# Performance work log

Measured on AMD Instinct MI355X. Metric: run time of the kernel, lower is better.

The kernel has to match this reference:

```python
import jax, jax.numpy as jnp
import numpy as np

DIM = 1536
DEPTH = 8
HEADS = 8
KV_HEADS = 1
GROUPS = HEADS // KV_HEADS
DQK = 128
DV = 192
DIM_PW = 128
POOL = 16
FF_INNER = int(DIM * 2.0)
SOFTCLAMP = 5.0
SCALE = 64 ** -0.5  # source uses default dim_head=64 for scale, not dim_head_qk
MAX_POS = 8192
EPS = float(jnp.finfo(jnp.float32).eps)


def rmsnorm(x, g):
    return x * jax.lax.rsqrt(jnp.mean(x * x, axis=-1, keepdims=True) + EPS) * g


def rotate_half(x):
    x1, x2 = jnp.split(x, 2, axis=-1)
    return jnp.concatenate([-x2, x1], axis=-1)


def apply_rope(pos, t):
    return t * jnp.cos(pos) + rotate_half(t) * jnp.sin(pos)


def rotary_emb(seq_len):
    nf = DQK // 2
    # torch.logspace(1, MAX_POS-nf+1, nf) = 10**linspace -> overflows to inf in fp32 (faithful)
    inv_freq = 1.0 / (jnp.arange(nf, dtype=jnp.float32) + 10.0 ** jnp.linspace(1.0, MAX_POS - nf + 1, nf, dtype=jnp.float32))
    freqs = jnp.arange(seq_len, dtype=jnp.float32)[:, None] * inv_freq[None, :]
    return jnp.concatenate([freqs, freqs], axis=-1)  # [n, DQK]


def softclamp(t, value=SOFTCLAMP):
    return jnp.tanh(t / value) * value


def attention(x, pairwise, rope, w_qkv, qg, kg, vg, bg, w_bias, w_out):
    b, n, _ = x.shape
    qkv = x @ w_qkv
    q, k, v = jnp.split(qkv, [HEADS * DQK, HEADS * DQK + DQK], axis=-1)
    # b n (g h d) -> b g h n d
    q = q.reshape(b, n, GROUPS, KV_HEADS, DQK).transpose(0, 2, 3, 1, 4)
    k = k.reshape(b, n, KV_HEADS, DQK).transpose(0, 2, 1, 3)
    v = v.reshape(b, n, KV_HEADS, DV).transpose(0, 2, 1, 3)
    q = rmsnorm(q, qg)
    k = rmsnorm(k, kg)
    v = rmsnorm(v, vg)
    q = q * SCALE
    q = apply_rope(rope, q)
    k = apply_rope(rope, k)
    sim = jnp.einsum('bghid,bhjd->bghij', q, k)
    # pairwise bias: RMSNorm -> GELU -> Linear(dim_pw, heads) -> b g h i j
    pb = jax.nn.gelu(rmsnorm(pairwise, bg), approximate=False) @ w_bias  # [b, i, j, heads]
    bi = pb.shape[1]
    bias = pb.reshape(b, bi, bi, GROUPS, KV_HEADS).transpose(0, 3, 4, 1, 2)
    bias = jnp.repeat(jnp.repeat(bias, POOL, axis=3), POOL, axis=4)  # expand to seq res
    sim = softclamp(sim + bias)
    attn = jax.nn.softmax(sim, axis=-1)
    out = jnp.einsum('bghij,bhjd->bghid', attn, v)
    out = out.transpose(0, 3, 1, 2, 4).reshape(b, n, GROUPS * KV_HEADS * DV)
    return out @ w_out


def tower(x, pairwise, w_qkv, q_gamma, k_gamma, v_gamma, bias_gamma, w_bias, w_out, attn_pre_gamma, ff_pre_gamma, w_ff1, b_ff1, w_ff2, b_ff2):
    rope = rotary_emb(x.shape[1])
    for d in range(DEPTH):
        xn = rmsnorm(x, attn_pre_gamma[d])
        x = x + attention(xn, pairwise, rope, w_qkv[d], q_gamma[d], k_gamma[d], v_gamma[d], bias_gamma[d], w_bias[d], w_out[d])
        xn = rmsnorm(x, ff_pre_gamma[d])
        x = x + (jax.nn.relu(xn @ w_ff1[d] + b_ff1[d]) @ w_ff2[d] + b_ff2[d])
    return x


def setup_inputs() -> dict:
    key = jax.random.key(0)
    ks = jax.random.split(key, 10)
    s = 0.02
    inp = {
        'x': jax.random.normal(ks[0], (2, 2048, DIM), jnp.float32),
        'pairwise': jax.random.normal(ks[1], (2, 128, 128, DIM_PW), jnp.float32),
        'w_qkv': jax.random.normal(ks[2], (DEPTH, DIM, HEADS * DQK + DQK + DV), jnp.float32) * s,
        'q_gamma': jnp.ones((DEPTH, DQK), jnp.float32),
        'k_gamma': jnp.ones((DEPTH, DQK), jnp.float32),
        'v_gamma': jnp.ones((DEPTH, DV), jnp.float32),
        'bias_gamma': jnp.ones((DEPTH, DIM_PW), jnp.float32),
        'w_bias': jax.random.normal(ks[3], (DEPTH, DIM_PW, HEADS), jnp.float32) * s,
        'w_out': jax.random.normal(ks[4], (DEPTH, DV * HEADS, DIM), jnp.float32) * s,
        'attn_pre_gamma': jnp.ones((DEPTH, DIM), jnp.float32),
        'ff_pre_gamma': jnp.ones((DEPTH, DIM), jnp.float32),
        'w_ff1': jax.random.normal(ks[5], (DEPTH, DIM, FF_INNER), jnp.float32) * s,
        'b_ff1': jnp.zeros((DEPTH, FF_INNER), jnp.float32),
        'w_ff2': jax.random.normal(ks[6], (DEPTH, FF_INNER, DIM), jnp.float32) * s,
        'b_ff2': jnp.zeros((DEPTH, DIM), jnp.float32),
    }
    return inp


def reference(x, pairwise, w_qkv, q_gamma, k_gamma, v_gamma, bias_gamma, w_bias, w_out, attn_pre_gamma, ff_pre_gamma, w_ff1, b_ff1, w_ff2, b_ff2):
    return tower(x, pairwise, w_qkv, q_gamma, k_gamma, v_gamma, bias_gamma, w_bias, w_out, attn_pre_gamma, ff_pre_gamma, w_ff1, b_ff1, w_ff2, b_ff2)
```

## Files before the change

### kernel.cpp

```cpp
#include <hip/hip_runtime.h>

typedef __bf16 bf16;
typedef float f32x4 __attribute__((ext_vector_type(4)));
typedef __bf16 bf16x8 __attribute__((ext_vector_type(8)));
typedef __bf16 bf16x4 __attribute__((ext_vector_type(4)));

#define EPSF 1.1920928955078125e-07f

#define GLOAD_LDS16(gsrc, ldst) \
  __builtin_amdgcn_global_load_lds((const __attribute__((address_space(1))) void*)(gsrc), \
                                   (__attribute__((address_space(3))) void*)(ldst), 16, 0, 0)

__device__ __forceinline__ float wave_reduce_sum(float v) {
#pragma unroll
  for (int m = 1; m < 64; m <<= 1) v += __shfl_xor(v, m, 64);
  return v;
}

__global__ __launch_bounds__(256) void wcast_t(const float* __restrict__ src,
                                               bf16* __restrict__ dst, int R, int C) {
  __shared__ float t[32][33];
  int z = blockIdx.z;
  const float* s = src + (size_t)z * R * C;
  bf16* d = dst + (size_t)z * R * C;
  int c0 = blockIdx.x * 32, r0 = blockIdx.y * 32;
  int tx = threadIdx.x, ty = threadIdx.y;
#pragma unroll
  for (int k = 0; k < 4; ++k)
    t[ty + k * 8][tx] = s[(size_t)(r0 + ty + k * 8) * C + c0 + tx];
  __syncthreads();
#pragma unroll
  for (int k = 0; k < 4; ++k)
    d[(size_t)(c0 + ty + k * 8) * R + r0 + tx] = (bf16)t[tx][ty + k * 8];
}

__global__ __launch_bounds__(256) void rmsnorm_k(const float* __restrict__ X,
                                                 const float* __restrict__ G,
                                                 bf16* __restrict__ O) {
  int row = blockIdx.x, tid = threadIdx.x, lane = tid & 63, w = tid >> 6;
  const float* x = X + (size_t)row * 1536;
  float v[6];
  float ss = 0.f;
#pragma unroll
  for (int k = 0; k < 6; ++k) { v[k] = x[tid + k * 256]; ss += v[k] * v[k]; }
  ss = wave_reduce_sum(ss);
  __shared__ float wsum[4];
  if (lane == 0) wsum[w] = ss;
  __syncthreads();
  ss = wsum[0] + wsum[1] + wsum[2] + wsum[3];
  float rs = rsqrtf(ss * (1.f / 1536.f) + EPSF);
  bf16* o = O + (size_t)row * 1536;
#pragma unroll
  for (int k = 0; k < 6; ++k) o[tid + k * 256] = (bf16)(v[k] * rs * G[tid + k * 256]);
}

template <int EPI>
__global__ __launch_bounds__(256, 3) void gemm_bt(const bf16* __restrict__ A,
                                                  const bf16* __restrict__ Bt,
                                                  float* __restrict__ Cf,
                                                  bf16* __restrict__ Cb,
                                                  const float* __restrict__ bias,
                                                  int M, int N, int K) {
  __shared__ __align__(16) char As[128 * 128];
  __shared__ __align__(16) char Bs[128 * 128];
  const int tid = threadIdx.x;
  const int lane = tid & 63, l15 = lane & 15, l4 = lane >> 4;
  const int w = tid >> 6;
  const int nwg = gridDim.x * gridDim.y;
  const int bid = blockIdx.y * gridDim.x + blockIdx.x;
  const int cpx = nwg >> 3;
  const int swz = (bid & 7) * cpx + (bid >> 3);
  const int rm = (swz / gridDim.x) * 128;
  const int cn = (swz % gridDim.x) * 128;
  const int wm = (w >> 1) * 64, wn = (w & 1) * 64;
  f32x4 acc[4][4] = {};

  for (int kk = 0; kk < K; kk += 64) {
#pragma unroll
    for (int r = 0; r < 4; ++r) {
      uint32_t o = (uint32_t)(r * 256 + tid) * 16;
      uint32_t row = o >> 7;
      uint32_t kb = ((o >> 4) & 7) ^ (row & 7);
      const bf16* src = A + (size_t)(rm + (int)row) * K + kk + kb * 8;
      GLOAD_LDS16(src, As + (o & 0xFFFFFC00u));
    }
#pragma unroll
    for (int r = 0; r < 4; ++r) {
      uint32_t o = (uint32_t)(r * 256 + tid) * 16;
      uint32_t row = o >> 7;
      uint32_t kb = ((o >> 4) & 7) ^ (row & 7);
      int nrow = cn + (int)row;
      if (nrow >= N) nrow = N - 1;
      const bf16* src = Bt + (size_t)nrow * K + kk + kb * 8;
      GLOAD_LDS16(src, Bs + (o & 0xFFFFFC00u));
    }
    __syncthreads();
#pragma unroll
    for (int s = 0; s < 2; ++s) {
      bf16x8 a[4], b[4];
#pragma unroll
      for (int m = 0; m < 4; ++m) {
        uint32_t row = wm + m * 16 + l15;
        uint32_t kb = (uint32_t)(s * 4 + l4);
        a[m] = *(const bf16x8*)(As + row * 128 + (kb ^ (row & 7)) * 16);
      }
#pragma unroll
      for (int n = 0; n < 4; ++n) {
        uint32_t row = wn + n * 16 + l15;
        uint32_t kb = (uint32_t)(s * 4 + l4);
        b[n] = *(const bf16x8*)(Bs + row * 128 + (kb ^ (row & 7)) * 16);
      }
      __builtin_amdgcn_s_setprio(1);
#pragma unroll
      for (int m = 0; m < 4; ++m)
#pragma unroll
        for (int n = 0; n < 4; ++n)
          acc[m][n] = __builtin_amdgcn_mfma_f32_16x16x32_bf16(a[m], b[n], acc[m][n], 0, 0, 0);
      __builtin_amdgcn_s_setprio(0);
    }
    __syncthreads();
  }

#pragma unroll
  for (int m = 0; m < 4; ++m)
#pragma unroll
    for (int n = 0; n < 4; ++n)
#pragma unroll
      for (int r = 0; r < 4; ++r) {
        int row = rm + wm + m * 16 + l4 * 4 + r;
        int col = cn + wn + n * 16 + l15;
        if (col < N) {
          float v = acc[m][n][r];
          size_t idx = (size_t)row * N + col;
          if constexpr (EPI == 0) {
            Cf[idx] = v;
          } else if constexpr (EPI == 2) {
            Cf[idx] += v;
          } else if constexpr (EPI == 3) {
            float tv = v + bias[col];
            Cb[idx] = (bf16)(tv > 0.f ? tv : 0.f);
          } else if constexpr (EPI == 4) {
            Cf[idx] += v + bias[col];
          }
        }
      }
}

template <int EPI>
__global__ __launch_bounds__(256, 4) void gemm_bt64(const bf16* __restrict__ A,
                                                    const bf16* __restrict__ Bt,
                                                    float* __restrict__ Cf,
                                                    bf16* __restrict__ Cb,
                                                    const float* __restrict__ bias,
                                                    int M, int N, int K) {
  __shared__ __align__(16) char As[64 * 128];
  __shared__ __align__(16) char Bs[128 * 128];
  const int tid = threadIdx.x;
  const int lane = tid & 63, l15 = lane & 15, l4 = lane >> 4;
  const int w = tid >> 6;
  const int nwg = gridDim.x * gridDim.y;
  const int bid = blockIdx.y * gridDim.x + blockIdx.x;
  const int cpx = nwg >> 3;
  const int swz = (bid & 7) * cpx + (bid >> 3);
  const int rm = (swz / gridDim.x) * 64;
  const int cn = (swz % gridDim.x) * 128;
  const int wm = (w >> 1) * 32, wn = (w & 1) * 64;
  f32x4 acc[2][4] = {};

  for (int kk = 0; kk < K; kk += 64) {
#pragma unroll
    for (int r = 0; r < 2; ++r) {
      uint32_t o = (uint32_t)(r * 256 + tid) * 16;
      uint32_t row = o >> 7;
      uint32_t kb = ((o >> 4) & 7) ^ (row & 7);
      const bf16* src = A + (size_t)(rm + (int)row) * K + kk + kb * 8;
      GLOAD_LDS16(src, As + (o & 0xFFFFFC00u));
    }
#pragma unroll
    for (int r = 0; r < 4; ++r) {
      uint32_t o = (uint32_t)(r * 256 + tid) * 16;
      uint32_t row = o >> 7;
      uint32_t kb = ((o >> 4) & 7) ^ (row & 7);
      int nrow = cn + (int)row;
      if (nrow >= N) nrow = N - 1;
      const bf16* src = Bt + (size_t)nrow * K + kk + kb * 8;
      GLOAD_LDS16(src, Bs + (o & 0xFFFFFC00u));
    }
    __syncthreads();
#pragma unroll
    for (int s = 0; s < 2; ++s) {
      bf16x8 a[2], b[4];
#pragma unroll
      for (int m = 0; m < 2; ++m) {
        uint32_t row = wm + m * 16 + l15;
        uint32_t kb = (uint32_t)(s * 4 + l4);
        a[m] = *(const bf16x8*)(As + row * 128 + (kb ^ (row & 7)) * 16);
      }
#pragma unroll
      for (int n = 0; n < 4; ++n) {
        uint32_t row = wn + n * 16 + l15;
        uint32_t kb = (uint32_t)(s * 4 + l4);
        b[n] = *(const bf16x8*)(Bs + row * 128 + (kb ^ (row & 7)) * 16);
      }
      __builtin_amdgcn_s_setprio(1);
#pragma unroll
      for (int m = 0; m < 2; ++m)
#pragma unroll
        for (int n = 0; n < 4; ++n)
          acc[m][n] = __builtin_amdgcn_mfma_f32_16x16x32_bf16(a[m], b[n], acc[m][n], 0, 0, 0);
      __builtin_amdgcn_s_setprio(0);
    }
    __syncthreads();
  }

#pragma unroll
  for (int m = 0; m < 2; ++m)
#pragma unroll
    for (int n = 0; n < 4; ++n)
#pragma unroll
      for (int r = 0; r < 4; ++r) {
        int row = rm + wm + m * 16 + l4 * 4 + r;
        int col = cn + wn + n * 16 + l15;
        if (col < N) {
          float v = acc[m][n][r];
          size_t idx = (size_t)row * N + col;
          if constexpr (EPI == 0) {
            Cf[idx] = v;
          } else if constexpr (EPI == 2) {
            Cf[idx] += v;
          } else if constexpr (EPI == 3) {
            float tv = v + bias[col];
            Cb[idx] = (bf16)(tv > 0.f ? tv : 0.f);
          } else if constexpr (EPI == 4) {
            Cf[idx] += v + bias[col];
          }
        }
      }
}

__global__ void qkv_post(const float* __restrict__ qkv, const float* __restrict__ qg,
                         const float* __restrict__ kg, const float* __restrict__ vg,
                         bf16* __restrict__ Qo, bf16* __restrict__ Ko, bf16* __restrict__ Vo) {
  int t = blockIdx.x, seg = blockIdx.y, lane = threadIdx.x;
  int b = t >> 11, n = t & 2047;
  const float* base;
  const float* gamma;
  int len;
  if (seg < 8) { base = qkv + (size_t)t * 1344 + seg * 128; gamma = qg; len = 128; }
  else if (seg == 8) { base = qkv + (size_t)t * 1344 + 1024; gamma = kg; len = 128; }
  else { base = qkv + (size_t)t * 1344 + 1152; gamma = vg; len = 192; }
  float v0 = base[lane], v1 = base[lane + 64];
  float v2 = (len == 192) ? base[lane + 128] : 0.f;
  float ss = wave_reduce_sum(v0 * v0 + v1 * v1 + v2 * v2);
  float rs = rsqrtf(ss / (float)len + EPSF);
  float n0 = v0 * rs * gamma[lane];
  float n1 = v1 * rs * gamma[lane + 64];
  if (seg < 8) {
    n0 *= 0.125f; n1 *= 0.125f;
    if (lane == 0) {
      float th = 0.1f * (float)n;
      float c = cosf(th), s_ = sinf(th);
      float r0 = n0 * c - n1 * s_, r1 = n1 * c + n0 * s_;
      n0 = r0; n1 = r1;
    }
    bf16* q = Qo + ((size_t)((b * 8 + seg) * 2048 + n)) * 128;
    q[lane] = (bf16)n0; q[lane + 64] = (bf16)n1;
  } else if (seg == 8) {
    if (lane == 0) {
      float th = 0.1f * (float)n;
      float c = cosf(th), s_ = sinf(th);
      float r0 = n0 * c - n1 * s_, r1 = n1 * c + n0 * s_;
      n0 = r0; n1 = r1;
    }
    bf16* k = Ko + ((size_t)(b * 2048 + n)) * 128;
    k[lane] = (bf16)n0; k[lane + 64] = (bf16)n1;
  } else {
    float n2 = v2 * rs * vg[lane + 128];
    bf16* vp = Vo + ((size_t)(b * 2048 + n)) * 192;
    vp[lane] = (bf16)n0; vp[lane + 64] = (bf16)n1; vp[lane + 128] = (bf16)n2;
  }
}

__global__ __launch_bounds__(256) void vtrans(const bf16* __restrict__ V, bf16* __restrict__ Vt) {
  __shared__ bf16 t[32][33];
  int b = blockIdx.z;
  int j0 = blockIdx.x * 32, d0 = blockIdx.y * 32;
  int tx = threadIdx.x, ty = threadIdx.y;
#pragma unroll
  for (int k = 0; k < 4; ++k)
    t[ty + k * 8][tx] = V[((size_t)b * 2048 + j0 + ty + k * 8) * 192 + d0 + tx];
  __syncthreads();
#pragma unroll
  for (int k = 0; k < 4; ++k)
    Vt[((size_t)b * 192 + d0 + ty + k * 8) * 2048 + j0 + tx] = t[tx][ty + k * 8];
}

__global__ void bias_pw(const float* __restrict__ P, const float* __restrict__ g,
                        const float* __restrict__ Wb, float* __restrict__ Bout) {
  int j = blockIdx.x, i = blockIdx.y, b = blockIdx.z;
  int lane = threadIdx.x;
  const float* p = P + (((size_t)b * 128 + i) * 128 + j) * 128;
  float a0 = p[lane], a1 = p[lane + 64];
  float ss = wave_reduce_sum(a0 * a0 + a1 * a1);
  float rs = rsqrtf(ss * (1.f / 128.f) + EPSF);
  float x0 = a0 * rs * g[lane], x1 = a1 * rs * g[lane + 64];
  float g0 = 0.5f * x0 * (1.f + erff(x0 * 0.70710678118654752f));
  float g1 = 0.5f * x1 * (1.f + erff(x1 * 0.70710678118654752f));
  __shared__ float gs[128];
  gs[lane] = g0; gs[lane + 64] = g1;
  __syncthreads();
  int h = lane & 7;
  float acc = 0.f;
#pragma unroll
  for (int k = 0; k < 16; ++k) {
    int c = (lane >> 3) + k * 8;
    acc += gs[c] * Wb[c * 8 + h];
  }
  acc += __shfl_xor(acc, 8, 64);
  acc += __shfl_xor(acc, 16, 64);
  acc += __shfl_xor(acc, 32, 64);
  if (lane < 8) Bout[(((size_t)b * 8 + lane) * 128 + i) * 128 + j] = acc;
}

__global__ __launch_bounds__(256, 2) void attn_k(const bf16* __restrict__ Q,
                                                 const bf16* __restrict__ Kg,
                                                 const bf16* __restrict__ Vt,
                                                 const float* __restrict__ Bias,
                                                 bf16* __restrict__ O0, bf16* __restrict__ O1,
                                                 float* __restrict__ L0, float* __restrict__ L1) {
  __shared__ __align__(16) char Ks[64 * 256];
  __shared__ __align__(16) char Vs[192 * 128];
  __shared__ __align__(16) char Ps[128 * 128];
  __shared__ float BiasS[8 * 128];
  int tid = threadIdx.x, lane = tid & 63, w = tid >> 6;
  int it = blockIdx.x, g = blockIdx.y, bz = blockIdx.z;
  int b = bz >> 1, js = bz & 1;
  bf16* __restrict__ Op = js ? O1 : O0;
  float* __restrict__ Lp = js ? L1 : L0;
  int i0 = it * 128;
  int l15 = lane & 15, l4 = lane >> 4;

  bf16x8 qf[2][4];
#pragma unroll
  for (int m = 0; m < 2; ++m)
#pragma unroll
    for (int s = 0; s < 4; ++s)
      qf[m][s] = *(const bf16x8*)(Q + ((size_t)((b * 8 + g) * 2048 + i0 + w * 32 + m * 16 + l15)) * 128 + s * 32 + l4 * 8);

  {
    int r = tid >> 5, c = (tid & 31) * 4;
    float4 bv = *(const float4*)(Bias + ((size_t)((b * 8 + g) * 128) + (i0 >> 4) + r) * 128 + c);
    bv.x *= 0.57707801635558535f; bv.y *= 0.57707801635558535f;
    bv.z *= 0.57707801635558535f; bv.w *= 0.57707801635558535f;
    *(float4*)&BiasS[r * 128 + c] = bv;
  }

  f32x4 accO[2][12] = {};
  float lacc[2] = {0.f, 0.f};

  for (int jt = js * 16; jt < js * 16 + 16; ++jt) {
    int j0 = jt * 64;
#pragma unroll
    for (int r = 0; r < 4; ++r) {
      uint32_t o = (uint32_t)(r * 256 + tid) * 16;
      uint32_t row = o >> 8;
      uint32_t kb = ((o >> 4) & 15) ^ (row & 15);
      const bf16* src = Kg + ((size_t)b * 2048 + j0 + (int)row) * 128 + kb * 8;
      GLOAD_LDS16(src, Ks + (o & 0xFFFFFC00u));
    }
#pragma unroll
    for (int r = 0; r < 6; ++r) {
      uint32_t o = (uint32_t)(r * 256 + tid) * 16;
      uint32_t dv = o >> 7;
      uint32_t kb = ((o >> 4) & 7) ^ (dv & 7);
      const bf16* src = Vt + ((size_t)b * 192 + dv) * 2048 + j0 + kb * 8;
      GLOAD_LDS16(src, Vs + (o & 0xFFFFFC00u));
    }
    __syncthreads();

    f32x4 accS[2][4] = {};
#pragma unroll
    for (int s = 0; s < 4; ++s) {
      bf16x8 kf[4];
#pragma unroll
      for (int n = 0; n < 4; ++n) {
        uint32_t row = n * 16 + l15;
        uint32_t kb = (uint32_t)(s * 4 + l4);
        kf[n] = *(const bf16x8*)(Ks + row * 256 + (kb ^ (row & 15)) * 16);
      }
      __builtin_amdgcn_s_setprio(1);
#pragma unroll
      for (int n = 0; n < 4; ++n)
#pragma unroll
        for (int m = 0; m < 2; ++m)
          accS[m][n] = __builtin_amdgcn_mfma_f32_16x16x32_bf16(kf[n], qf[m][s], accS[m][n], 0, 0, 0);
      __builtin_amdgcn_s_setprio(0);
    }

#pragma unroll
    for (int m = 0; m < 2; ++m) {
#pragma unroll
      for (int n = 0; n < 4; ++n) {
        float biaS = BiasS[(w * 2 + m) * 128 + jt * 4 + n];
        bf16x4 pk;
#pragma unroll
        for (int r = 0; r < 4; ++r) {
          float t1 = __builtin_fmaf(0.57707801635558535f, accS[m][n][r], biaS);
          float e1 = exp2f(t1);
          float rr = __builtin_amdgcn_rcpf(e1 + 1.0f);
          float pv = exp2f(-14.426950408889634f * rr);
          lacc[m] += pv;
          pk[r] = (bf16)pv;
        }
        uint32_t prow = (uint32_t)(w * 32 + m * 16 + l15);
        uint32_t byteo = prow * 128 + (uint32_t)(n * 16 + l4 * 4) * 2;
        byteo ^= (prow & 7) << 4;
        *(bf16x4*)(Ps + byteo) = pk;
      }
    }

#pragma unroll
    for (int s = 0; s < 2; ++s) {
      bf16x8 pa[2];
#pragma unroll
      for (int m = 0; m < 2; ++m) {
        uint32_t row = (uint32_t)(w * 32 + m * 16 + l15);
        uint32_t byteo = row * 128 + (uint32_t)(s * 64 + l4 * 16);
        byteo ^= (row & 7) << 4;
        pa[m] = *(const bf16x8*)(Ps + byteo);
      }
#pragma unroll
      for (int n = 0; n < 12; ++n) {
        uint32_t dvr = n * 16 + l15;
        uint32_t kb = (uint32_t)(s * 4 + l4);
        bf16x8 vf = *(const bf16x8*)(Vs + dvr * 128 + (kb ^ (dvr & 7)) * 16);
        __builtin_amdgcn_s_setprio(1);
#pragma unroll
        for (int m = 0; m < 2; ++m)
          accO[m][n] = __builtin_amdgcn_mfma_f32_16x16x32_bf16(vf, pa[m], accO[m][n], 0, 0, 0);
        __builtin_amdgcn_s_setprio(0);
      }
    }
    __syncthreads();
  }

#pragma unroll
  for (int m = 0; m < 2; ++m) {
    float l = lacc[m];
    l += __shfl_xor(l, 16, 64);
    l += __shfl_xor(l, 32, 64);
    lacc[m] = l;
  }
  if (l4 == 0) {
#pragma unroll
    for (int m = 0; m < 2; ++m)
      Lp[(size_t)(b * 8 + g) * 2048 + i0 + w * 32 + m * 16 + l15] = lacc[m];
  }

#pragma unroll
  for (int m = 0; m < 2; ++m) {
    int i = i0 + w * 32 + m * 16 + l15;
#pragma unroll
    for (int n = 0; n < 12; ++n) {
      bf16x4 ok;
#pragma unroll
      for (int r = 0; r < 4; ++r) ok[r] = (bf16)accO[m][n][r];
      int dv = n * 16 + l4 * 4;
      *(bf16x4*)(Op + ((size_t)(b * 8 + g) * 2048 + i) * 192 + dv) = ok;
    }
  }
}

__global__ __launch_bounds__(256) void attn_cmb(const bf16* __restrict__ O0,
                                                const bf16* __restrict__ O1,
                                                const float* __restrict__ L0,
                                                const float* __restrict__ L1,
                                                bf16* __restrict__ Out) {
  size_t e = ((size_t)blockIdx.x * 256u + threadIdx.x) * 8u;
  uint32_t dv = (uint32_t)(e % 192u);
  uint32_t rest = (uint32_t)(e / 192u);
  uint32_t i = rest & 2047u;
  uint32_t g = (rest >> 11) & 7u;
  uint32_t b = rest >> 14;
  bf16x8 a = *(const bf16x8*)(O0 + e);
  bf16x8 c = *(const bf16x8*)(O1 + e);
  float rl = __builtin_amdgcn_rcpf(L0[rest] + L1[rest]);
  bf16x8 t;
#pragma unroll
  for (int k = 0; k < 8; ++k) t[k] = (bf16)(((float)a[k] + (float)c[k]) * rl);
  *(bf16x8*)(Out + ((size_t)(b * 2048 + i)) * 1536 + g * 192 + dv) = t;
}

extern "C" void kernel_launch(void* const* d_in, const int* in_sizes, int n_in,
                              void* d_out, int out_size, void* d_ws, size_t ws_size,
                              hipStream_t stream) {
  (void)in_sizes; (void)n_in; (void)out_size;
  const float* x_in = (const float*)d_in[0];
  const float* pairwise = (const float*)d_in[1];
  const float* w_qkv = (const float*)d_in[2];
  const float* q_gamma = (const float*)d_in[3];
  const float* k_gamma = (const float*)d_in[4];
  const float* v_gamma = (const float*)d_in[5];
  const float* bias_gamma = (const float*)d_in[6];
  const float* w_bias = (const float*)d_in[7];
  const float* w_out = (const float*)d_in[8];
  const float* attn_pre = (const float*)d_in[9];
  const float* ff_pre = (const float*)d_in[10];
  const float* w_ff1 = (const float*)d_in[11];
  const float* b_ff1 = (const float*)d_in[12];
  const float* w_ff2 = (const float*)d_in[13];
  const float* b_ff2 = (const float*)d_in[14];

  char* p = (char*)d_ws;
  auto alloc = [&](size_t bytes) {
    char* r = p;
    p += (bytes + 255) & ~(size_t)255;
    return r;
  };
  bf16* wT_qkv = (bf16*)alloc(8ull * 1344 * 1536 * 2);
  bf16* wT_out = (bf16*)alloc(8ull * 1536 * 1536 * 2);
  bf16* wT_ff1 = (bf16*)alloc(8ull * 3072 * 1536 * 2);
  bf16* wT_ff2 = (bf16*)alloc(8ull * 1536 * 3072 * 2);
  float* x_ws = (float*)alloc(4096ull * 1536 * 4);
  bf16* xn = (bf16*)alloc(4096ull * 1536 * 2);
  float* qkvb = (float*)alloc(4096ull * 1344 * 4);
  bf16* qb = (bf16*)alloc(2ull * 8 * 2048 * 128 * 2);
  bf16* kb = (bf16*)alloc(2ull * 2048 * 128 * 2);
  bf16* vb = (bf16*)alloc(2ull * 2048 * 192 * 2);
  bf16* vtb = (bf16*)alloc(2ull * 192 * 2048 * 2);
  float* biasb = (float*)alloc(2ull * 8 * 128 * 128 * 4);
  bf16* attn_o = (bf16*)alloc(4096ull * 1536 * 2);
  bf16* hb = (bf16*)alloc(4096ull * 3072 * 2);
  bf16* op0 = (bf16*)alloc(2ull * 8 * 2048 * 192 * 2);
  bf16* op1 = (bf16*)alloc(2ull * 8 * 2048 * 192 * 2);
  float* lp0 = (float*)alloc(2ull * 8 * 2048 * 4);
  float* lp1 = (float*)alloc(2ull * 8 * 2048 * 4);
  if ((size_t)(p - (char*)d_ws) > ws_size) return;

  wcast_t<<<dim3(42, 48, 8), dim3(32, 8), 0, stream>>>(w_qkv, wT_qkv, 1536, 1344);
  wcast_t<<<dim3(48, 48, 8), dim3(32, 8), 0, stream>>>(w_out, wT_out, 1536, 1536);
  wcast_t<<<dim3(96, 48, 8), dim3(32, 8), 0, stream>>>(w_ff1, wT_ff1, 1536, 3072);
  wcast_t<<<dim3(48, 96, 8), dim3(32, 8), 0, stream>>>(w_ff2, wT_ff2, 3072, 1536);

  hipMemcpyAsync(x_ws, x_in, 4096ull * 1536 * 4, hipMemcpyDeviceToDevice, stream);

  for (int d = 0; d < 8; ++d) {
    const bf16* wq = wT_qkv + (size_t)d * 1344 * 1536;
    const bf16* wo = wT_out + (size_t)d * 1536 * 1536;
    const bf16* w1 = wT_ff1 + (size_t)d * 3072 * 1536;
    const bf16* w2 = wT_ff2 + (size_t)d * 1536 * 3072;

    rmsnorm_k<<<4096, 256, 0, stream>>>(x_ws, attn_pre + d * 1536, xn);
    gemm_bt64<0><<<dim3(11, 64), 256, 0, stream>>>(xn, wq, qkvb, nullptr, nullptr, 4096, 1344, 1536);
    qkv_post<<<dim3(4096, 10), 64, 0, stream>>>(qkvb, q_gamma + d * 128, k_gamma + d * 128,
                                                v_gamma + d * 192, qb, kb, vb);
    vtrans<<<dim3(64, 6, 2), dim3(32, 8), 0, stream>>>(vb, vtb);
    bias_pw<<<dim3(128, 128, 2), 64, 0, stream>>>(pairwise, bias_gamma + d * 128,
                                                  w_bias + d * 128 * 8, biasb);
    attn_k<<<dim3(16, 8, 4), 256, 0, stream>>>(qb, kb, vtb, biasb, op0, op1, lp0, lp1);
    attn_cmb<<<3072, 256, 0, stream>>>(op0, op1, lp0, lp1, attn_o);
    gemm_bt64<2><<<dim3(12, 64), 256, 0, stream>>>(attn_o, wo, x_ws, nullptr, nullptr, 4096, 1536, 1536);
    rmsnorm_k<<<4096, 256, 0, stream>>>(x_ws, ff_pre + d * 1536, xn);
    gemm_bt<3><<<dim3(24, 32), 256, 0, stream>>>(xn, w1, nullptr, hb, b_ff1 + d * 3072, 4096, 3072, 1536);
    gemm_bt64<4><<<dim3(12, 64), 256, 0, stream>>>(hb, w2, x_ws, nullptr, b_ff2 + d * 1536, 4096, 1536, 3072);
  }

  hipMemcpyAsync(d_out, x_ws, 4096ull * 1536 * 4, hipMemcpyDeviceToDevice, stream);
}
```

Before: 2.551 ms.

## Drop split-KV attention in favour of 64-row query tiles over full sequence

The attention kernel no longer splits the key range into two halves with a separate combine kernel. Each block now handles 64 query rows (16 per wave) across all 32 key tiles and normalises by the row sum in the epilogue, writing straight into the final layout. This removes the partial-output round trip through global memory and one kernel launch, and occupancy is raised to 3 blocks per CU. The block count stays the same, but each block does half as many MFMAs per K/V tile load, so K/V reuse drops and load traffic per unit of compute doubles.

New measurement: 2.475 ms. 1.03x faster.

```diff
diff --git a/kernel.cpp b/kernel.cpp
--- a/kernel.cpp
+++ b/kernel.cpp
@@ -322,32 +322,26 @@
   if (lane < 8) Bout[(((size_t)b * 8 + lane) * 128 + i) * 128 + j] = acc;
 }
 
-__global__ __launch_bounds__(256, 2) void attn_k(const bf16* __restrict__ Q,
+__global__ __launch_bounds__(256, 3) void attn_k(const bf16* __restrict__ Q,
                                                  const bf16* __restrict__ Kg,
                                                  const bf16* __restrict__ Vt,
                                                  const float* __restrict__ Bias,
-                                                 bf16* __restrict__ O0, bf16* __restrict__ O1,
-                                                 float* __restrict__ L0, float* __restrict__ L1) {
+                                                 bf16* __restrict__ Out) {
   __shared__ __align__(16) char Ks[64 * 256];
   __shared__ __align__(16) char Vs[192 * 128];
-  __shared__ __align__(16) char Ps[128 * 128];
-  __shared__ float BiasS[8 * 128];
+  __shared__ __align__(16) char Ps[64 * 128];
+  __shared__ float BiasS[4 * 128];
   int tid = threadIdx.x, lane = tid & 63, w = tid >> 6;
-  int it = blockIdx.x, g = blockIdx.y, bz = blockIdx.z;
-  int b = bz >> 1, js = bz & 1;
-  bf16* __restrict__ Op = js ? O1 : O0;
-  float* __restrict__ Lp = js ? L1 : L0;
-  int i0 = it * 128;
+  int it = blockIdx.x, g = blockIdx.y, b = blockIdx.z;
+  int i0 = it * 64;
   int l15 = lane & 15, l4 = lane >> 4;
 
-  bf16x8 qf[2][4];
-#pragma unroll
-  for (int m = 0; m < 2; ++m)
-#pragma unroll
-    for (int s = 0; s < 4; ++s)
-      qf[m][s] = *(const bf16x8*)(Q + ((size_t)((b * 8 + g) * 2048 + i0 + w * 32 + m * 16 + l15)) * 128 + s * 32 + l4 * 8);
-
-  {
+  bf16x8 qf[4];
+#pragma unroll
+  for (int s = 0; s < 4; ++s)
+    qf[s] = *(const bf16x8*)(Q + ((size_t)((b * 8 + g) * 2048 + i0 + w * 16 + l15)) * 128 + s * 32 + l4 * 8);
+
+  if (tid < 128) {
     int r = tid >> 5, c = (tid & 31) * 4;
     float4 bv = *(const float4*)(Bias + ((size_t)((b * 8 + g) * 128) + (i0 >> 4) + r) * 128 + c);
     bv.x *= 0.57707801635558535f; bv.y *= 0.57707801635558535f;
@@ -355,10 +349,10 @@
     *(float4*)&BiasS[r * 128 + c] = bv;
   }
 
-  f32x4 accO[2][12] = {};
-  float lacc[2] = {0.f, 0.f};
-
-  for (int jt = js * 16; jt < js * 16 + 16; ++jt) {
+  f32x4 accO[12] = {};
+  float lacc = 0.f;
+
+  for (int jt = 0; jt < 32; ++jt) {
     int j0 = jt * 64;
 #pragma unroll
     for (int r = 0; r < 4; ++r) {
@@ -378,7 +372,7 @@
     }
     __syncthreads();
 
-    f32x4 accS[2][4] = {};
+    f32x4 accS[4] = {};
 #pragma unroll
     for (int s = 0; s < 4; ++s) {
       bf16x8 kf[4];
@@ -391,104 +385,63 @@
       __builtin_amdgcn_s_setprio(1);
 #pragma unroll
       for (int n = 0; n < 4; ++n)
-#pragma unroll
-        for (int m = 0; m < 2; ++m)
-          accS[m][n] = __builtin_amdgcn_mfma_f32_16x16x32_bf16(kf[n], qf[m][s], accS[m][n], 0, 0, 0);
+        accS[n] = __builtin_amdgcn_mfma_f32_16x16x32_bf16(kf[n], qf[s], accS[n], 0, 0, 0);
       __builtin_amdgcn_s_setprio(0);
     }
 
 #pragma unroll
-    for (int m = 0; m < 2; ++m) {
-#pragma unroll
-      for (int n = 0; n < 4; ++n) {
-        float biaS = BiasS[(w * 2 + m) * 128 + jt * 4 + n];
-        bf16x4 pk;
-#pragma unroll
-        for (int r = 0; r < 4; ++r) {
-          float t1 = __builtin_fmaf(0.57707801635558535f, accS[m][n][r], biaS);
-          float e1 = exp2f(t1);
-          float rr = __builtin_amdgcn_rcpf(e1 + 1.0f);
-          float pv = exp2f(-14.426950408889634f * rr);
-          lacc[m] += pv;
-          pk[r] = (bf16)pv;
-        }
-        uint32_t prow = (uint32_t)(w * 32 + m * 16 + l15);
-        uint32_t byteo = prow * 128 + (uint32_t)(n * 16 + l4 * 4) * 2;
-        byteo ^= (prow & 7) << 4;
-        *(bf16x4*)(Ps + byteo) = pk;
-      }
+    for (int n = 0; n < 4; ++n) {
+      float biaS = BiasS[w * 128 + jt * 4 + n];
+      bf16x4 pk;
+#pragma unroll
+      for (int r = 0; r < 4; ++r) {
+        float t1 = __builtin_fmaf(0.57707801635558535f, accS[n][r], biaS);
+        float e1 = exp2f(t1);
+        float rr = __builtin_amdgcn_rcpf(e1 + 1.0f);
+        float pv = exp2f(-14.426950408889634f * rr);
+        lacc += pv;
+        pk[r] = (bf16)pv;
+      }
+      uint32_t prow = (uint32_t)(w * 16 + l15);
+      uint32_t byteo = prow * 128 + (uint32_t)(n * 16 + l4 * 4) * 2;
+      byteo ^= (prow & 7) << 4;
+      *(bf16x4*)(Ps + byteo) = pk;
     }
 
 #pragma unroll
     for (int s = 0; s < 2; ++s) {
-      bf16x8 pa[2];
-#pragma unroll
-      for (int m = 0; m < 2; ++m) {
-        uint32_t row = (uint32_t)(w * 32 + m * 16 + l15);
-        uint32_t byteo = row * 128 + (uint32_t)(s * 64 + l4 * 16);
-        byteo ^= (row & 7) << 4;
-        pa[m] = *(const bf16x8*)(Ps + byteo);
-      }
+      uint32_t prow = (uint32_t)(w * 16 + l15);
+      uint32_t byteo = prow * 128 + (uint32_t)(s * 64 + l4 * 16);
+      byteo ^= (prow & 7) << 4;
+      bf16x8 pa = *(const bf16x8*)(Ps + byteo);
 #pragma unroll
       for (int n = 0; n < 12; ++n) {
         uint32_t dvr = n * 16 + l15;
         uint32_t kb = (uint32_t)(s * 4 + l4);
         bf16x8 vf = *(const bf16x8*)(Vs + dvr * 128 + (kb ^ (dvr & 7)) * 16);
         __builtin_amdgcn_s_setprio(1);
-#pragma unroll
-        for (int m = 0; m < 2; ++m)
-          accO[m][n] = __builtin_amdgcn_mfma_f32_16x16x32_bf16(vf, pa[m], accO[m][n], 0, 0, 0);
+        accO[n] = __builtin_amdgcn_mfma_f32_16x16x32_bf16(vf, pa, accO[n], 0, 0, 0);
         __builtin_amdgcn_s_setprio(0);
       }
     }
     __syncthreads();
   }
 
-#pragma unroll
-  for (int m = 0; m < 2; ++m) {
-    float l = lacc[m];
-    l += __shfl_xor(l, 16, 64);
-    l += __shfl_xor(l, 32, 64);
-    lacc[m] = l;
-  }
-  if (l4 == 0) {
-#pragma unroll
-    for (int m = 0; m < 2; ++m)
-      Lp[(size_t)(b * 8 + g) * 2048 + i0 + w * 32 + m * 16 + l15] = lacc[m];
-  }
-
-#pragma unroll
-  for (int m = 0; m < 2; ++m) {
-    int i = i0 + w * 32 + m * 16 + l15;
+  lacc += __shfl_xor(lacc, 16, 64);
+  lacc += __shfl_xor(lacc, 32, 64);
+  float rl = __builtin_amdgcn_rcpf(lacc);
+
+  {
+    int i = i0 + w * 16 + l15;
 #pragma unroll
     for (int n = 0; n < 12; ++n) {
       bf16x4 ok;
 #pragma unroll
-      for (int r = 0; r < 4; ++r) ok[r] = (bf16)accO[m][n][r];
+      for (int r = 0; r < 4; ++r) ok[r] = (bf16)(accO[n][r] * rl);
       int dv = n * 16 + l4 * 4;
-      *(bf16x4*)(Op + ((size_t)(b * 8 + g) * 2048 + i) * 192 + dv) = ok;
-    }
-  }
-}
-
-__global__ __launch_bounds__(256) void attn_cmb(const bf16* __restrict__ O0,
-                                                const bf16* __restrict__ O1,
-                                                const float* __restrict__ L0,
-                                                const float* __restrict__ L1,
-                                                bf16* __restrict__ Out) {
-  size_t e = ((size_t)blockIdx.x * 256u + threadIdx.x) * 8u;
-  uint32_t dv = (uint32_t)(e % 192u);
-  uint32_t rest = (uint32_t)(e / 192u);
-  uint32_t i = rest & 2047u;
-  uint32_t g = (rest >> 11) & 7u;
-  uint32_t b = rest >> 14;
-  bf16x8 a = *(const bf16x8*)(O0 + e);
-  bf16x8 c = *(const bf16x8*)(O1 + e);
-  float rl = __builtin_amdgcn_rcpf(L0[rest] + L1[rest]);
-  bf16x8 t;
-#pragma unroll
-  for (int k = 0; k < 8; ++k) t[k] = (bf16)(((float)a[k] + (float)c[k]) * rl);
-  *(bf16x8*)(Out + ((size_t)(b * 2048 + i)) * 1536 + g * 192 + dv) = t;
+      *(bf16x4*)(Out + ((size_t)(b * 2048 + i)) * 1536 + g * 192 + dv) = ok;
+    }
+  }
 }
 
 extern "C" void kernel_launch(void* const* d_in, const int* in_sizes, int n_in,
@@ -531,10 +484,6 @@
   float* biasb = (float*)alloc(2ull * 8 * 128 * 128 * 4);
   bf16* attn_o = (bf16*)alloc(4096ull * 1536 * 2);
   bf16* hb = (bf16*)alloc(4096ull * 3072 * 2);
-  bf16* op0 = (bf16*)alloc(2ull * 8 * 2048 * 192 * 2);
-  bf16* op1 = (bf16*)alloc(2ull * 8 * 2048 * 192 * 2);
-  float* lp0 = (float*)alloc(2ull * 8 * 2048 * 4);
-  float* lp1 = (float*)alloc(2ull * 8 * 2048 * 4);
   if ((size_t)(p - (char*)d_ws) > ws_size) return;
 
   wcast_t<<<dim3(42, 48, 8), dim3(32, 8), 0, stream>>>(w_qkv, wT_qkv, 1536, 1344);
@@ -557,8 +506,7 @@
     vtrans<<<dim3(64, 6, 2), dim3(32, 8), 0, stream>>>(vb, vtb);
     bias_pw<<<dim3(128, 128, 2), 64, 0, stream>>>(pairwise, bias_gamma + d * 128,
                                                   w_bias + d * 128 * 8, biasb);
-    attn_k<<<dim3(16, 8, 4), 256, 0, stream>>>(qb, kb, vtb, biasb, op0, op1, lp0, lp1);
-    attn_cmb<<<3072, 256, 0, stream>>>(op0, op1, lp0, lp1, attn_o);
+    attn_k<<<dim3(32, 8, 2), 256, 0, stream>>>(qb, kb, vtb, biasb, attn_o);
     gemm_bt64<2><<<dim3(12, 64), 256, 0, stream>>>(attn_o, wo, x_ws, nullptr, nullptr, 4096, 1536, 1536);
     rmsnorm_k<<<4096, 256, 0, stream>>>(x_ws, ff_pre + d * 1536, xn);
     gemm_bt<3><<<dim3(24, 32), 256, 0, stream>>>(xn, w1, nullptr, hb, b_ff1 + d * 3072, 4096, 3072, 1536);
```
